# Kernel tuning notes

Measured on AMD Instinct MI355X. Metric: run time of the kernel, lower is better.

The kernel has to match this reference:

```python
import jax, jax.numpy as jnp
import numpy as np

NUM_CODE = 20000
EMBED_DIM = 256
B, V, C = 64, 50, 64
HALF = EMBED_DIM // 2


def setup_inputs() -> dict:
    key = jax.random.key(0)
    k1, k2, k3, k4, k5, k6 = jax.random.split(key, 6)
    input_code = jax.random.randint(k1, (B, V, C), 0, NUM_CODE, dtype=jnp.int64)
    length_code = jax.random.randint(k2, (B, V), 0, C, dtype=jnp.int64)
    embed_table = jax.random.normal(k3, (NUM_CODE, EMBED_DIM), dtype=jnp.float32)
    embed_table = embed_table.at[0].set(0.0)  # padding_idx=0
    # Linear(D, D//2) and Linear(D//2, 1), torch-style y = x @ W.T + b
    lim1 = 1.0 / np.sqrt(EMBED_DIM)
    W1 = jax.random.uniform(k4, (HALF, EMBED_DIM), jnp.float32, -lim1, lim1)
    b1 = jnp.zeros((HALF,), jnp.float32)
    lim2 = 1.0 / np.sqrt(HALF)
    W2 = jax.random.uniform(k5, (1, HALF), jnp.float32, -lim2, lim2)
    b2 = jnp.zeros((1,), jnp.float32)
    return {"input_code": input_code, "length_code": length_code,
            "embed_table": embed_table, "W1": W1, "b1": b1, "W2": W2, "b2": b2}


def reference(input_code, length_code, embed_table, W1, b1, W2, b2):
    nb, nv, nc = input_code.shape
    length = length_code.reshape(nb * nv)  # [BV]
    mask = jnp.arange(nc)[None, :] < length[:, None]  # [BV, C]
    emb = embed_table[input_code].reshape(nb * nv, nc, -1)  # [BV, C, D]
    # attention scores: Linear -> tanh -> Linear
    h = jnp.tanh(jnp.einsum('bcd,hd->bch', emb, W1) + b1)  # [BV, C, H]
    w = jnp.einsum('bch,oh->bco', h, W2) + b2               # [BV, C, 1]
    w = jnp.where(mask[:, :, None], w, -1e9)
    attn = jax.nn.softmax(w, axis=1)                         # [BV, C, 1]
    out = jnp.einsum('bco,bcd->bd', attn, emb)               # [BV, D]
    return out.reshape(nb, nv, -1)
```

## Files before the change

kernel.cpp:

```cpp
#include <hip/hip_runtime.h>
#include <math.h>

#define NUM_CODE 20000
#define EMBED_D  256
#define HID      128
#define CC       64
#define NBV      3200

typedef __attribute__((ext_vector_type(8))) short bf16x8;
typedef __attribute__((ext_vector_type(4))) float f32x4;

__device__ __forceinline__ unsigned f2bf1(float f) {
    union { float f; unsigned u; } c; c.f = f;
    return (c.u + 0x7FFFu + ((c.u >> 16) & 1u)) >> 16;
}
__device__ __forceinline__ unsigned pk2(float lo, float hi) {
    return f2bf1(lo) | (f2bf1(hi) << 16);
}
__device__ __forceinline__ float bflo(unsigned u) {
    union { unsigned u; float f; } c; c.u = u << 16; return c.f;
}
__device__ __forceinline__ float bfhi(unsigned u) {
    union { unsigned u; float f; } c; c.u = u & 0xFFFF0000u; return c.f;
}

__global__ __launch_bounds__(256) void w1_cvt(
    const float* __restrict__ W1, unsigned short* __restrict__ W1b)
{
    int f = blockIdx.x * 256 + threadIdx.x;
    float4 v = ((const float4*)W1)[f];
    uint2 o; o.x = pk2(v.x, v.y); o.y = pk2(v.z, v.w);
    ((uint2*)W1b)[f] = o;
}

__global__ __launch_bounds__(64) void score_mfma(
    const float* __restrict__ table, const unsigned short* __restrict__ W1b,
    const float* __restrict__ b1, const float* __restrict__ W2,
    const float* __restrict__ b2, float* __restrict__ scores,
    unsigned short* __restrict__ tbl_bf, int write_bf)
{
    const int l   = threadIdx.x;
    const int row = l & 15;
    const int kg  = l >> 4;
    const int m0  = blockIdx.x * 16;
    const float* arow = table + (size_t)(m0 + row) * EMBED_D + kg * 8;

    f32x4 acc[8];
#pragma unroll
    for (int j = 0; j < 8; j++) acc[j] = (f32x4){0.f, 0.f, 0.f, 0.f};

    float4 a0 = *(const float4*)(arow);
    float4 a1 = *(const float4*)(arow + 4);

#pragma unroll
    for (int s = 0; s < 8; s++) {
        float4 n0, n1;
        if (s < 7) {
            n0 = *(const float4*)(arow + (s + 1) * 32);
            n1 = *(const float4*)(arow + (s + 1) * 32 + 4);
        }
        union { uint4 u; bf16x8 v; } p;
        p.u.x = pk2(a0.x, a0.y); p.u.y = pk2(a0.z, a0.w);
        p.u.z = pk2(a1.x, a1.y); p.u.w = pk2(a1.z, a1.w);
        if (write_bf)
            *(uint4*)(tbl_bf + (size_t)(m0 + row) * EMBED_D + s * 32 + kg * 8) = p.u;
#pragma unroll
        for (int j = 0; j < 8; j++) {
            bf16x8 bf = *(const bf16x8*)(W1b + (size_t)(j * 16 + row) * EMBED_D + s * 32 + kg * 8);
            acc[j] = __builtin_amdgcn_mfma_f32_16x16x32_bf16(p.v, bf, acc[j], 0, 0, 0);
        }
        a0 = n0; a1 = n1;
    }

    float w2v[8], b1v[8];
#pragma unroll
    for (int j = 0; j < 8; j++) {
        w2v[j] = W2[j * 16 + row];
        b1v[j] = b1[j * 16 + row];
    }
#pragma unroll
    for (int r = 0; r < 4; r++) {
        float part = 0.f;
#pragma unroll
        for (int j = 0; j < 8; j++)
            part += w2v[j] * tanhf(acc[j][r] + b1v[j]);
#pragma unroll
        for (int o = 1; o < 16; o <<= 1)
            part += __shfl_xor(part, o, 16);
        if (row == 0)
            scores[m0 + kg * 4 + r] = part + b2[0];
    }
}

__global__ __launch_bounds__(256) void attn_v3(
    const int* __restrict__ codes, const int* __restrict__ lens,
    const uint4* __restrict__ t16, const float* __restrict__ scores,
    float* __restrict__ out)
{
    __shared__ float attn_s[CC];
    __shared__ int   code_s[CC];
    __shared__ float red[8][256];

    const int bv  = blockIdx.x;
    const int tid = threadIdx.x;
    const int g   = tid >> 5;
    const int l   = tid & 31;

    int c_reg = 0;
    if (tid < CC) {
        c_reg = codes[(size_t)bv * CC + tid];
        code_s[tid] = c_reg;
    }
    __syncthreads();

    uint4 v[8];
#pragma unroll
    for (int cc = 0; cc < 8; cc++)
        v[cc] = t16[(size_t)code_s[cc * 8 + g] * 32 + l];

    if (tid < CC) {
        float sc  = scores[c_reg];
        int   len = lens[bv];
        float val = (tid < len) ? sc : -1e9f;
        float m = val;
#pragma unroll
        for (int o = 32; o >= 1; o >>= 1)
            m = fmaxf(m, __shfl_xor(m, o, 64));
        float e = expf(val - m);
        float sum = e;
#pragma unroll
        for (int o = 32; o >= 1; o >>= 1)
            sum += __shfl_xor(sum, o, 64);
        attn_s[tid] = e / sum;
    }
    __syncthreads();

    float acc[8] = {0.f, 0.f, 0.f, 0.f, 0.f, 0.f, 0.f, 0.f};
#pragma unroll
    for (int cc = 0; cc < 8; cc++) {
        float a = attn_s[cc * 8 + g];
        unsigned u;
        u = v[cc].x; acc[0] += a * bflo(u); acc[1] += a * bfhi(u);
        u = v[cc].y; acc[2] += a * bflo(u); acc[3] += a * bfhi(u);
        u = v[cc].z; acc[4] += a * bflo(u); acc[5] += a * bfhi(u);
        u = v[cc].w; acc[6] += a * bflo(u); acc[7] += a * bfhi(u);
    }
#pragma unroll
    for (int e = 0; e < 8; e++) red[g][l * 8 + e] = acc[e];
    __syncthreads();

    if (tid < 64) {
        float4 o = make_float4(0.f, 0.f, 0.f, 0.f);
#pragma unroll
        for (int g2 = 0; g2 < 8; g2++) {
            float4 r = *(const float4*)&red[g2][tid * 4];
            o.x += r.x; o.y += r.y; o.z += r.z; o.w += r.w;
        }
        ((float4*)out)[(size_t)bv * 64 + tid] = o;
    }
}

__global__ __launch_bounds__(256) void attn_f32(
    const int* __restrict__ codes, const int* __restrict__ lens,
    const float* __restrict__ table, const float* __restrict__ scores,
    float* __restrict__ out)
{
    __shared__ float attn_s[CC];
    __shared__ int   code_s[CC];
    __shared__ float4 red4[3][64];

    const int bv  = blockIdx.x;
    const int tid = threadIdx.x;

    if (tid < CC) {
        int c = codes[(size_t)bv * CC + tid];
        code_s[tid] = c;
        float sc  = scores[c];
        int   len = lens[bv];
        float val = (tid < len) ? sc : -1e9f;
        float m = val;
#pragma unroll
        for (int o = 32; o >= 1; o >>= 1)
            m = fmaxf(m, __shfl_xor(m, o, 64));
        float e = expf(val - m);
        float sum = e;
#pragma unroll
        for (int o = 32; o >= 1; o >>= 1)
            sum += __shfl_xor(sum, o, 64);
        attn_s[tid] = e / sum;
    }
    __syncthreads();

    const int g = tid >> 6;
    const int l = tid & 63;
    const float4* t4 = (const float4*)table;
    float4 acc = make_float4(0.f, 0.f, 0.f, 0.f);
#pragma unroll
    for (int cc = 0; cc < 16; cc++) {
        int c   = cc * 4 + g;
        float a = attn_s[c];
        float4 vv = t4[(size_t)code_s[c] * 64 + l];
        acc.x += a * vv.x; acc.y += a * vv.y; acc.z += a * vv.z; acc.w += a * vv.w;
    }
    if (g > 0) red4[g - 1][l] = acc;
    __syncthreads();
    if (g == 0) {
#pragma unroll
        for (int r = 0; r < 3; r++) {
            float4 vv = red4[r][l];
            acc.x += vv.x; acc.y += vv.y; acc.z += vv.z; acc.w += vv.w;
        }
        ((float4*)out)[(size_t)bv * 64 + l] = acc;
    }
}

extern "C" void kernel_launch(void* const* d_in, const int* in_sizes, int n_in,
                              void* d_out, int out_size, void* d_ws, size_t ws_size,
                              hipStream_t stream) {
    const int*   input_code  = (const int*)d_in[0];
    const int*   length_code = (const int*)d_in[1];
    const float* embed_table = (const float*)d_in[2];
    const float* W1 = (const float*)d_in[3];
    const float* b1 = (const float*)d_in[4];
    const float* W2 = (const float*)d_in[5];
    const float* b2 = (const float*)d_in[6];
    float* out = (float*)d_out;

    float*          scores = (float*)d_ws;
    unsigned short* W1b    = (unsigned short*)((char*)d_ws + 81920);
    unsigned short* tbl_bf = (unsigned short*)((char*)d_ws + 81920 + 65536);
    const size_t need_full = 81920 + 65536 + (size_t)NUM_CODE * EMBED_D * 2;
    const int use_bf = (ws_size >= need_full) ? 1 : 0;

    w1_cvt<<<32, 256, 0, stream>>>(W1, W1b);
    score_mfma<<<NUM_CODE / 16, 64, 0, stream>>>(
        embed_table, W1b, b1, W2, b2, scores, tbl_bf, use_bf);
    if (use_bf)
        attn_v3<<<NBV, 256, 0, stream>>>(input_code, length_code,
                                         (const uint4*)tbl_bf, scores, out);
    else
        attn_f32<<<NBV, 256, 0, stream>>>(input_code, length_code,
                                          embed_table, scores, out);
}
```

Measured before the change: 109.7 us.

## Split score MFMA hidden columns across four waves and reduce through LDS

The score kernel now runs 512-thread blocks that cover 32 codes. Each group of four waves splits the 128 hidden units, so every wave holds two accumulators instead of eight and issues a quarter of the MFMAs. Partial tanh·W2 sums are combined through shared memory, and the score is written as a float4. The aim is more wave-level parallelism and lower register pressure on the table-scoring pass. The cost is that each table row is loaded and converted to bf16 four times, plus an added barrier. The attention kernel also writes its reduction buffer with vector float4 stores instead of scalar stores.

```diff
diff --git a/kernel.cpp b/kernel.cpp
--- a/kernel.cpp
+++ b/kernel.cpp
@@ -33,21 +33,28 @@
     ((uint2*)W1b)[f] = o;
 }
 
-__global__ __launch_bounds__(64) void score_mfma(
+__global__ __launch_bounds__(512) void score_mfma2(
     const float* __restrict__ table, const unsigned short* __restrict__ W1b,
     const float* __restrict__ b1, const float* __restrict__ W2,
     const float* __restrict__ b2, float* __restrict__ scores,
     unsigned short* __restrict__ tbl_bf, int write_bf)
 {
-    const int l   = threadIdx.x;
-    const int row = l & 15;
-    const int kg  = l >> 4;
-    const int m0  = blockIdx.x * 16;
+    __shared__ float comb[2][3][64 * 5];
+
+    const int tid  = threadIdx.x;
+    const int wave = tid >> 6;
+    const int t    = wave >> 2;
+    const int jg   = wave & 3;
+    const int l    = tid & 63;
+    const int row  = l & 15;
+    const int kg   = l >> 4;
+    const int m0   = blockIdx.x * 32 + t * 16;
+
     const float* arow = table + (size_t)(m0 + row) * EMBED_D + kg * 8;
 
-    f32x4 acc[8];
-#pragma unroll
-    for (int j = 0; j < 8; j++) acc[j] = (f32x4){0.f, 0.f, 0.f, 0.f};
+    f32x4 acc[2];
+    acc[0] = (f32x4){0.f, 0.f, 0.f, 0.f};
+    acc[1] = (f32x4){0.f, 0.f, 0.f, 0.f};
 
     float4 a0 = *(const float4*)(arow);
     float4 a1 = *(const float4*)(arow + 4);
@@ -62,37 +69,58 @@
         union { uint4 u; bf16x8 v; } p;
         p.u.x = pk2(a0.x, a0.y); p.u.y = pk2(a0.z, a0.w);
         p.u.z = pk2(a1.x, a1.y); p.u.w = pk2(a1.z, a1.w);
-        if (write_bf)
+        if (write_bf && jg == 0)
             *(uint4*)(tbl_bf + (size_t)(m0 + row) * EMBED_D + s * 32 + kg * 8) = p.u;
 #pragma unroll
-        for (int j = 0; j < 8; j++) {
+        for (int jj = 0; jj < 2; jj++) {
+            int j = jg * 2 + jj;
             bf16x8 bf = *(const bf16x8*)(W1b + (size_t)(j * 16 + row) * EMBED_D + s * 32 + kg * 8);
-            acc[j] = __builtin_amdgcn_mfma_f32_16x16x32_bf16(p.v, bf, acc[j], 0, 0, 0);
+            acc[jj] = __builtin_amdgcn_mfma_f32_16x16x32_bf16(p.v, bf, acc[jj], 0, 0, 0);
         }
         a0 = n0; a1 = n1;
     }
 
-    float w2v[8], b1v[8];
-#pragma unroll
-    for (int j = 0; j < 8; j++) {
-        w2v[j] = W2[j * 16 + row];
-        b1v[j] = b1[j * 16 + row];
-    }
-#pragma unroll
-    for (int r = 0; r < 4; r++) {
-        float part = 0.f;
-#pragma unroll
-        for (int j = 0; j < 8; j++)
-            part += w2v[j] * tanhf(acc[j][r] + b1v[j]);
-#pragma unroll
-        for (int o = 1; o < 16; o <<= 1)
-            part += __shfl_xor(part, o, 16);
-        if (row == 0)
-            scores[m0 + kg * 4 + r] = part + b2[0];
-    }
-}
-
-__global__ __launch_bounds__(256) void attn_v3(
+    float part[4];
+#pragma unroll
+    for (int r = 0; r < 4; r++) part[r] = 0.f;
+#pragma unroll
+    for (int jj = 0; jj < 2; jj++) {
+        int j = jg * 2 + jj;
+        float w2 = W2[j * 16 + row];
+        float bb = b1[j * 16 + row];
+#pragma unroll
+        for (int r = 0; r < 4; r++)
+            part[r] += w2 * tanhf(acc[jj][r] + bb);
+    }
+
+    if (jg != 0) {
+#pragma unroll
+        for (int r = 0; r < 4; r++)
+            comb[t][jg - 1][l * 5 + r] = part[r];
+    }
+    __syncthreads();
+    if (jg == 0) {
+#pragma unroll
+        for (int g2 = 0; g2 < 3; g2++)
+#pragma unroll
+            for (int r = 0; r < 4; r++)
+                part[r] += comb[t][g2][l * 5 + r];
+#pragma unroll
+        for (int r = 0; r < 4; r++) {
+#pragma unroll
+            for (int o = 1; o < 16; o <<= 1)
+                part[r] += __shfl_xor(part[r], o, 16);
+        }
+        if (row == 0) {
+            float b2v = b2[0];
+            float4 o4 = make_float4(part[0] + b2v, part[1] + b2v,
+                                    part[2] + b2v, part[3] + b2v);
+            *(float4*)&scores[m0 + kg * 4] = o4;
+        }
+    }
+}
+
+__global__ __launch_bounds__(256) void attn_v4(
     const int* __restrict__ codes, const int* __restrict__ lens,
     const uint4* __restrict__ t16, const float* __restrict__ scores,
     float* __restrict__ out)
@@ -145,8 +173,8 @@
         u = v[cc].z; acc[4] += a * bflo(u); acc[5] += a * bfhi(u);
         u = v[cc].w; acc[6] += a * bflo(u); acc[7] += a * bfhi(u);
     }
-#pragma unroll
-    for (int e = 0; e < 8; e++) red[g][l * 8 + e] = acc[e];
+    *(float4*)&red[g][l * 8]     = make_float4(acc[0], acc[1], acc[2], acc[3]);
+    *(float4*)&red[g][l * 8 + 4] = make_float4(acc[4], acc[5], acc[6], acc[7]);
     __syncthreads();
 
     if (tid < 64) {
@@ -233,10 +261,10 @@
     const int use_bf = (ws_size >= need_full) ? 1 : 0;
 
     w1_cvt<<<32, 256, 0, stream>>>(W1, W1b);
-    score_mfma<<<NUM_CODE / 16, 64, 0, stream>>>(
+    score_mfma2<<<NUM_CODE / 32, 512, 0, stream>>>(
         embed_table, W1b, b1, W2, b2, scores, tbl_bf, use_bf);
     if (use_bf)
-        attn_v3<<<NBV, 256, 0, stream>>>(input_code, length_code,
+        attn_v4<<<NBV, 256, 0, stream>>>(input_code, length_code,
                                          (const uint4*)tbl_bf, scores, out);
     else
         attn_f32<<<NBV, 256, 0, stream>>>(input_code, length_code,
```

Result: slower. 115.7 us (+5.5%).

## Fuse per-bag score MFMA into attention kernel and pre-convert table to bf16

Applied to the files above, without the earlier changes.

Replaces the global per-code score pass with a standalone conversion kernel that writes a bf16 copy of the table and W1. The attention kernel then stages each bag's 64 gathered rows in shared memory and computes the tanh-MLP scores there with MFMA. This removes one launch and the scores round trip, and it drops b2 because softmax is shift-invariant. In exchange, rows that recur across bags are rescored, about ten times the MFMA work of the old pass, and every wave re-reads all of W1b from global memory. It also switches to an exp-based fast tanh and drops the fp32 fallback path for small workspaces.

```diff
diff --git a/kernel.cpp b/kernel.cpp
--- a/kernel.cpp
+++ b/kernel.cpp
@@ -23,94 +23,53 @@
 __device__ __forceinline__ float bfhi(unsigned u) {
     union { unsigned u; float f; } c; c.u = u & 0xFFFF0000u; return c.f;
 }
-
-__global__ __launch_bounds__(256) void w1_cvt(
-    const float* __restrict__ W1, unsigned short* __restrict__ W1b)
-{
-    int f = blockIdx.x * 256 + threadIdx.x;
-    float4 v = ((const float4*)W1)[f];
-    uint2 o; o.x = pk2(v.x, v.y); o.y = pk2(v.z, v.w);
-    ((uint2*)W1b)[f] = o;
+__device__ __forceinline__ float tanh_fast(float x) {
+    float t = __expf(2.0f * x);
+    return 1.0f - 2.0f / (1.0f + t);
 }
 
-__global__ __launch_bounds__(64) void score_mfma(
-    const float* __restrict__ table, const unsigned short* __restrict__ W1b,
-    const float* __restrict__ b1, const float* __restrict__ W2,
-    const float* __restrict__ b2, float* __restrict__ scores,
-    unsigned short* __restrict__ tbl_bf, int write_bf)
+__global__ __launch_bounds__(256) void cvt_kernel(
+    const float* __restrict__ table, const float* __restrict__ W1,
+    unsigned short* __restrict__ tbl_bf, unsigned short* __restrict__ W1b)
 {
-    const int l   = threadIdx.x;
-    const int row = l & 15;
-    const int kg  = l >> 4;
-    const int m0  = blockIdx.x * 16;
-    const float* arow = table + (size_t)(m0 + row) * EMBED_D + kg * 8;
-
-    f32x4 acc[8];
-#pragma unroll
-    for (int j = 0; j < 8; j++) acc[j] = (f32x4){0.f, 0.f, 0.f, 0.f};
-
-    float4 a0 = *(const float4*)(arow);
-    float4 a1 = *(const float4*)(arow + 4);
-
-#pragma unroll
-    for (int s = 0; s < 8; s++) {
-        float4 n0, n1;
-        if (s < 7) {
-            n0 = *(const float4*)(arow + (s + 1) * 32);
-            n1 = *(const float4*)(arow + (s + 1) * 32 + 4);
-        }
-        union { uint4 u; bf16x8 v; } p;
-        p.u.x = pk2(a0.x, a0.y); p.u.y = pk2(a0.z, a0.w);
-        p.u.z = pk2(a1.x, a1.y); p.u.w = pk2(a1.z, a1.w);
-        if (write_bf)
-            *(uint4*)(tbl_bf + (size_t)(m0 + row) * EMBED_D + s * 32 + kg * 8) = p.u;
-#pragma unroll
-        for (int j = 0; j < 8; j++) {
-            bf16x8 bf = *(const bf16x8*)(W1b + (size_t)(j * 16 + row) * EMBED_D + s * 32 + kg * 8);
-            acc[j] = __builtin_amdgcn_mfma_f32_16x16x32_bf16(p.v, bf, acc[j], 0, 0, 0);
-        }
-        a0 = n0; a1 = n1;
-    }
-
-    float w2v[8], b1v[8];
-#pragma unroll
-    for (int j = 0; j < 8; j++) {
-        w2v[j] = W2[j * 16 + row];
-        b1v[j] = b1[j * 16 + row];
-    }
-#pragma unroll
-    for (int r = 0; r < 4; r++) {
-        float part = 0.f;
-#pragma unroll
-        for (int j = 0; j < 8; j++)
-            part += w2v[j] * tanhf(acc[j][r] + b1v[j]);
-#pragma unroll
-        for (int o = 1; o < 16; o <<= 1)
-            part += __shfl_xor(part, o, 16);
-        if (row == 0)
-            scores[m0 + kg * 4 + r] = part + b2[0];
+    int b = blockIdx.x;
+    if (b < 5000) {
+        int f = b * 256 + threadIdx.x;
+        float4 v = ((const float4*)table)[f];
+        uint2 o; o.x = pk2(v.x, v.y); o.y = pk2(v.z, v.w);
+        ((uint2*)tbl_bf)[f] = o;
+    } else {
+        int f = (b - 5000) * 256 + threadIdx.x;
+        float4 v = ((const float4*)W1)[f];
+        uint2 o; o.x = pk2(v.x, v.y); o.y = pk2(v.z, v.w);
+        ((uint2*)W1b)[f] = o;
     }
 }
 
-__global__ __launch_bounds__(256) void attn_v3(
+__global__ __launch_bounds__(256, 4) void fused_kernel(
     const int* __restrict__ codes, const int* __restrict__ lens,
-    const uint4* __restrict__ t16, const float* __restrict__ scores,
+    const uint4* __restrict__ t16, const unsigned short* __restrict__ W1b,
+    const float* __restrict__ b1, const float* __restrict__ W2,
     float* __restrict__ out)
 {
+    __shared__ uint4 smem4[2112];
+    __shared__ int   code_s[CC];
+    __shared__ float wrow[CC];
     __shared__ float attn_s[CC];
-    __shared__ int   code_s[CC];
-    __shared__ float red[8][256];
+
+    unsigned short* emb = (unsigned short*)smem4;
+    float*          red = (float*)smem4;
 
     const int bv  = blockIdx.x;
     const int tid = threadIdx.x;
     const int g   = tid >> 5;
     const int l   = tid & 31;
+    const int l6  = tid & 63;
+    const int w   = tid >> 6;
+    const int row = l6 & 15;
+    const int kg  = l6 >> 4;
 
-    int c_reg = 0;
-    if (tid < CC) {
-        c_reg = codes[(size_t)bv * CC + tid];
-        code_s[tid] = c_reg;
-    }
+    if (tid < CC) code_s[tid] = codes[(size_t)bv * CC + tid];
     __syncthreads();
 
     uint4 v[8];
@@ -118,10 +77,51 @@
     for (int cc = 0; cc < 8; cc++)
         v[cc] = t16[(size_t)code_s[cc * 8 + g] * 32 + l];
 
+#pragma unroll
+    for (int cc = 0; cc < 8; cc++) {
+        int c = cc * 8 + g;
+        *(uint4*)&emb[c * 264 + l * 8] = v[cc];
+    }
+    __syncthreads();
+
+    f32x4 acc[8];
+#pragma unroll
+    for (int j = 0; j < 8; j++) acc[j] = (f32x4){0.f, 0.f, 0.f, 0.f};
+#pragma unroll
+    for (int s = 0; s < 8; s++) {
+        bf16x8 afrag = *(const bf16x8*)&emb[(16 * w + row) * 264 + s * 32 + kg * 8];
+#pragma unroll
+        for (int j = 0; j < 8; j++) {
+            bf16x8 bw = *(const bf16x8*)&W1b[(size_t)(j * 16 + row) * EMBED_D + s * 32 + kg * 8];
+            acc[j] = __builtin_amdgcn_mfma_f32_16x16x32_bf16(afrag, bw, acc[j], 0, 0, 0);
+        }
+    }
+
+    float part[4] = {0.f, 0.f, 0.f, 0.f};
+#pragma unroll
+    for (int j = 0; j < 8; j++) {
+        float w2 = W2[j * 16 + row];
+        float bb = b1[j * 16 + row];
+#pragma unroll
+        for (int r = 0; r < 4; r++)
+            part[r] += w2 * tanh_fast(acc[j][r] + bb);
+    }
+#pragma unroll
+    for (int r = 0; r < 4; r++) {
+#pragma unroll
+        for (int o = 1; o < 16; o <<= 1)
+            part[r] += __shfl_xor(part[r], o, 16);
+    }
+    if (row == 0) {
+#pragma unroll
+        for (int r = 0; r < 4; r++)
+            wrow[16 * w + kg * 4 + r] = part[r];
+    }
+    __syncthreads();
+
     if (tid < CC) {
-        float sc  = scores[c_reg];
-        int   len = lens[bv];
-        float val = (tid < len) ? sc : -1e9f;
+        int len = lens[bv];
+        float val = (tid < len) ? wrow[tid] : -1e9f;
         float m = val;
 #pragma unroll
         for (int o = 32; o >= 1; o >>= 1)
@@ -135,110 +135,47 @@
     }
     __syncthreads();
 
-    float acc[8] = {0.f, 0.f, 0.f, 0.f, 0.f, 0.f, 0.f, 0.f};
+    float a2[8] = {0.f, 0.f, 0.f, 0.f, 0.f, 0.f, 0.f, 0.f};
 #pragma unroll
     for (int cc = 0; cc < 8; cc++) {
         float a = attn_s[cc * 8 + g];
         unsigned u;
-        u = v[cc].x; acc[0] += a * bflo(u); acc[1] += a * bfhi(u);
-        u = v[cc].y; acc[2] += a * bflo(u); acc[3] += a * bfhi(u);
-        u = v[cc].z; acc[4] += a * bflo(u); acc[5] += a * bfhi(u);
-        u = v[cc].w; acc[6] += a * bflo(u); acc[7] += a * bfhi(u);
+        u = v[cc].x; a2[0] += a * bflo(u); a2[1] += a * bfhi(u);
+        u = v[cc].y; a2[2] += a * bflo(u); a2[3] += a * bfhi(u);
+        u = v[cc].z; a2[4] += a * bflo(u); a2[5] += a * bfhi(u);
+        u = v[cc].w; a2[6] += a * bflo(u); a2[7] += a * bfhi(u);
     }
-#pragma unroll
-    for (int e = 0; e < 8; e++) red[g][l * 8 + e] = acc[e];
+    *(float4*)&red[g * 256 + l * 8]     = make_float4(a2[0], a2[1], a2[2], a2[3]);
+    *(float4*)&red[g * 256 + l * 8 + 4] = make_float4(a2[4], a2[5], a2[6], a2[7]);
     __syncthreads();
 
     if (tid < 64) {
         float4 o = make_float4(0.f, 0.f, 0.f, 0.f);
 #pragma unroll
         for (int g2 = 0; g2 < 8; g2++) {
-            float4 r = *(const float4*)&red[g2][tid * 4];
+            float4 r = *(const float4*)&red[g2 * 256 + tid * 4];
             o.x += r.x; o.y += r.y; o.z += r.z; o.w += r.w;
         }
         ((float4*)out)[(size_t)bv * 64 + tid] = o;
     }
 }
 
-__global__ __launch_bounds__(256) void attn_f32(
-    const int* __restrict__ codes, const int* __restrict__ lens,
-    const float* __restrict__ table, const float* __restrict__ scores,
-    float* __restrict__ out)
-{
-    __shared__ float attn_s[CC];
-    __shared__ int   code_s[CC];
-    __shared__ float4 red4[3][64];
-
-    const int bv  = blockIdx.x;
-    const int tid = threadIdx.x;
-
-    if (tid < CC) {
-        int c = codes[(size_t)bv * CC + tid];
-        code_s[tid] = c;
-        float sc  = scores[c];
-        int   len = lens[bv];
-        float val = (tid < len) ? sc : -1e9f;
-        float m = val;
-#pragma unroll
-        for (int o = 32; o >= 1; o >>= 1)
-            m = fmaxf(m, __shfl_xor(m, o, 64));
-        float e = expf(val - m);
-        float sum = e;
-#pragma unroll
-        for (int o = 32; o >= 1; o >>= 1)
-            sum += __shfl_xor(sum, o, 64);
-        attn_s[tid] = e / sum;
-    }
-    __syncthreads();
-
-    const int g = tid >> 6;
-    const int l = tid & 63;
-    const float4* t4 = (const float4*)table;
-    float4 acc = make_float4(0.f, 0.f, 0.f, 0.f);
-#pragma unroll
-    for (int cc = 0; cc < 16; cc++) {
-        int c   = cc * 4 + g;
-        float a = attn_s[c];
-        float4 vv = t4[(size_t)code_s[c] * 64 + l];
-        acc.x += a * vv.x; acc.y += a * vv.y; acc.z += a * vv.z; acc.w += a * vv.w;
-    }
-    if (g > 0) red4[g - 1][l] = acc;
-    __syncthreads();
-    if (g == 0) {
-#pragma unroll
-        for (int r = 0; r < 3; r++) {
-            float4 vv = red4[r][l];
-            acc.x += vv.x; acc.y += vv.y; acc.z += vv.z; acc.w += vv.w;
-        }
-        ((float4*)out)[(size_t)bv * 64 + l] = acc;
-    }
-}
-
 extern "C" void kernel_launch(void* const* d_in, const int* in_sizes, int n_in,
                               void* d_out, int out_size, void* d_ws, size_t ws_size,
                               hipStream_t stream) {
-    const int*   input_code  = (const int*)d_in[0];
-    const int*   length_code = (const int*)d_in[1];
-    const float* embed_table = (const float*)d_in[2];
+    const int*   codes = (const int*)d_in[0];
+    const int*   lens  = (const int*)d_in[1];
+    const float* table = (const float*)d_in[2];
     const float* W1 = (const float*)d_in[3];
     const float* b1 = (const float*)d_in[4];
     const float* W2 = (const float*)d_in[5];
-    const float* b2 = (const float*)d_in[6];
     float* out = (float*)d_out;
 
-    float*          scores = (float*)d_ws;
-    unsigned short* W1b    = (unsigned short*)((char*)d_ws + 81920);
-    unsigned short* tbl_bf = (unsigned short*)((char*)d_ws + 81920 + 65536);
-    const size_t need_full = 81920 + 65536 + (size_t)NUM_CODE * EMBED_D * 2;
-    const int use_bf = (ws_size >= need_full) ? 1 : 0;
+    unsigned short* tbl_bf = (unsigned short*)d_ws;
+    unsigned short* W1b    = (unsigned short*)((char*)d_ws
+                              + (size_t)NUM_CODE * EMBED_D * 2);
 
-    w1_cvt<<<32, 256, 0, stream>>>(W1, W1b);
-    score_mfma<<<NUM_CODE / 16, 64, 0, stream>>>(
-        embed_table, W1b, b1, W2, b2, scores, tbl_bf, use_bf);
-    if (use_bf)
-        attn_v3<<<NBV, 256, 0, stream>>>(input_code, length_code,
-                                         (const uint4*)tbl_bf, scores, out);
-    else
-        attn_f32<<<NBV, 256, 0, stream>>>(input_code, length_code,
-                                          embed_table, scores, out);
+    cvt_kernel<<<5032, 256, 0, stream>>>(table, W1, tbl_bf, W1b);
+    fused_kernel<<<NBV, 256, 0, stream>>>(codes, lens, (const uint4*)tbl_bf,
+                                          W1b, b1, W2, out);
 }
```

Result: slower. 195.7 us (+78.4%).
